# Kernel optimization log

Hardware: AMD Instinct MI355X
Metric: run time of the kernel (lower is better)

## Reference

```python
import jax, jax.numpy as jnp
import numpy as np
from jax import lax

B, T, D, H = 64, 1024, 256, 512


def setup_inputs() -> dict:
    key = jax.random.key(0)
    k1, k2, k3, k4, k5 = jax.random.split(key, 5)
    s = 1.0 / np.sqrt(H)
    return {
        "x": jax.random.normal(k1, (B, T, D), dtype=jnp.float32),
        "W_ih": jax.random.uniform(k2, (4 * H, D), minval=-s, maxval=s, dtype=jnp.float32),
        "W_hh": jax.random.uniform(k3, (4 * H, H), minval=-s, maxval=s, dtype=jnp.float32),
        "b_ih": jax.random.uniform(k4, (4 * H,), minval=-s, maxval=s, dtype=jnp.float32),
        "b_hh": jax.random.uniform(k5, (4 * H,), minval=-s, maxval=s, dtype=jnp.float32),
    }


def reference(x, W_ih, W_hh, b_ih, b_hh):
    # x: [B, T, D] -> time-major [T, B, D]
    xT = jnp.swapaxes(x, 0, 1)
    b, h_dim = x.shape[0], W_hh.shape[1]
    # Precompute input projections for all timesteps: [T, B, 4H]
    x_proj = jnp.einsum("tbd,gd->tbg", xT, W_ih) + b_ih + b_hh

    def step(carry, xg):
        h, c = carry
        gates = xg + h @ W_hh.T  # [B, 4H]
        i, f, g, o = jnp.split(gates, 4, axis=-1)
        c = jax.nn.sigmoid(f) * c + jax.nn.sigmoid(i) * jnp.tanh(g)
        h = jax.nn.sigmoid(o) * jnp.tanh(c)
        return (h, c), jax.nn.sigmoid(h)

    h0 = jnp.zeros((b, h_dim), dtype=x.dtype)
    c0 = jnp.zeros((b, h_dim), dtype=x.dtype)
    _, outs = lax.scan(step, (h0, c0), x_proj)  # outs: [T, B, H]
    # torch.cat along dim 0 over timesteps -> [T*B, H]
    return outs.reshape(-1, h_dim)
```

## Files before the change

### kernel.cpp

```cpp
#include <hip/hip_runtime.h>
#include <stdint.h>

#define T_STEPS 1024
#define BATCH   64
#define DIN     256
#define HDIM    512
#define G4      2048
#define NGRP    8
#define GWG     32
#define GB      8
#define NBUF    16

#define OFF_XCNT  0
#define OFF_ARR   128
#define OFF_BIAS  4096
#define OFF_WHH   16384
#define OFF_WIH   (16384 + G4*HDIM*2)
#define OFF_H     (OFF_WIH + G4*DIN*2)

typedef __attribute__((ext_vector_type(8))) short bf16x8;
typedef __attribute__((ext_vector_type(4))) float f32x4;

__device__ __forceinline__ unsigned short f2bf(float f) {
  union { float f; unsigned u; } v; v.f = f;
  unsigned r = v.u + 0x7FFF + ((v.u >> 16) & 1);
  return (unsigned short)(r >> 16);
}
__device__ __forceinline__ float sigm(float x)   { return 1.0f / (1.0f + __expf(-x)); }
__device__ __forceinline__ float tanh_f(float x) { return 2.0f / (1.0f + __expf(-2.0f * x)) - 1.0f; }

__global__ void k_init(unsigned char* ws) {
  int tid = blockIdx.x * blockDim.x + threadIdx.x;
  unsigned* w32 = (unsigned*)ws;
  if (tid < 512) w32[tid] = 0;
}

__global__ void k_pack(const float* __restrict__ W_ih, const float* __restrict__ W_hh,
                       const float* __restrict__ b_ih, const float* __restrict__ b_hh,
                       unsigned char* ws) {
  unsigned short* whh = (unsigned short*)(ws + OFF_WHH);
  unsigned short* wih = (unsigned short*)(ws + OFF_WIH);
  float* bias = (float*)(ws + OFF_BIAS);
  int tid = blockIdx.x * blockDim.x + threadIdx.x;
  int np = gridDim.x * blockDim.x;
  for (int i = tid; i < G4 * HDIM; i += np) whh[i] = f2bf(W_hh[i]);
  for (int i = tid; i < G4 * DIN;  i += np) wih[i] = f2bf(W_ih[i]);
  for (int i = tid; i < G4;        i += np) bias[i] = b_ih[i] + b_hh[i];
}

__device__ __forceinline__ void stage_x(const float* __restrict__ x, unsigned short* A_s,
                                        int g, int m, int c, int tstep) {
  const float* xb = x + ((size_t)(g * GB + m) * 1024 + tstep) * 256 + c * 8;
  float4 f0 = *(const float4*)(xb);
  float4 f1 = *(const float4*)(xb + 4);
  union { bf16x8 v; unsigned short s[8]; } u;
  u.s[0] = f2bf(f0.x); u.s[1] = f2bf(f0.y); u.s[2] = f2bf(f0.z); u.s[3] = f2bf(f0.w);
  u.s[4] = f2bf(f1.x); u.s[5] = f2bf(f1.y); u.s[6] = f2bf(f1.z); u.s[7] = f2bf(f1.w);
  *(bf16x8*)(A_s + m * 776 + 512 + c * 8) = u.v;
}

__global__ __launch_bounds__(256, 1) void k_lstm(unsigned char* ws,
                                                 const float* __restrict__ x,
                                                 float* __restrict__ out) {
  __shared__ __attribute__((aligned(16))) unsigned short A_s[16 * 776];
  __shared__ __attribute__((aligned(16))) unsigned short Whh_s[64 * 520];
  __shared__ __attribute__((aligned(16))) unsigned short Wih_s[64 * 264];
  __shared__ __attribute__((aligned(16))) float gl[16 * 64];
  __shared__ int s_rank;

  const int tid = threadIdx.x;

  unsigned xcc;
  asm("s_getreg_b32 %0, hwreg(HW_REG_XCC_ID)" : "=s"(xcc));
  xcc &= 7;
  unsigned* xcnt = (unsigned*)(ws + OFF_XCNT);
  if (tid == 0)
    s_rank = (int)__hip_atomic_fetch_add(&xcnt[xcc], 1u, __ATOMIC_RELAXED, __HIP_MEMORY_SCOPE_AGENT);
  __syncthreads();
  const int rank = s_rank;
  if (rank >= GWG) return;

  const int g  = (int)xcc;
  const int jt = rank;

  const unsigned short* whh_g = (const unsigned short*)(ws + OFF_WHH);
  const unsigned short* wih_g = (const unsigned short*)(ws + OFF_WIH);
  const float*          bias_g = (const float*)(ws + OFF_BIAS);
  unsigned short*       hring = (unsigned short*)(ws + OFF_H) + (size_t)g * (NBUF * GB * HDIM);
  unsigned* arrive = (unsigned*)(ws + OFF_ARR + g * 128);

  {
    int rl = tid >> 2, part = tid & 3;
    int grow = (rl >> 4) * 512 + jt * 16 + (rl & 15);
    const unsigned short* src = whh_g + grow * 512 + part * 128;
    unsigned short* dst = Whh_s + rl * 520 + part * 128;
    #pragma unroll
    for (int i = 0; i < 16; ++i) *(bf16x8*)(dst + i * 8) = *(const bf16x8*)(src + i * 8);
    const unsigned short* src2 = wih_g + grow * 256 + part * 64;
    unsigned short* dst2 = Wih_s + rl * 264 + part * 64;
    #pragma unroll
    for (int i = 0; i < 8; ++i) *(bf16x8*)(dst2 + i * 8) = *(const bf16x8*)(src2 + i * 8);
  }

  {
    unsigned* a32 = (unsigned*)A_s;
    for (int i = tid; i < 16 * 776 / 2; i += 256) a32[i] = 0;
  }

  float biasr[4];
  float c_reg = 0.f;
  const int ub = tid >> 4, jl = tid & 15;
  if (tid < 128) {
    #pragma unroll
    for (int gt = 0; gt < 4; ++gt)
      biasr[gt] = bias_g[gt * 512 + jt * 16 + jl];
  }

  const int lane = tid & 63, wave = tid >> 6;
  const int arow = lane & 15;
  const int kg   = (lane >> 4) * 8;
  const int rl   = wave * 16 + (lane & 15);
  const int sm   = tid >> 5, sc = tid & 31;

  __syncthreads();

  stage_x(x, A_s, g, sm, sc, 0);
  __syncthreads();
  f32x4 accX = {0.f, 0.f, 0.f, 0.f};
  #pragma unroll
  for (int kx = 0; kx < 8; ++kx) {
    bf16x8 a = *(const bf16x8*)(A_s + arow * 776 + 512 + kx * 32 + kg);
    bf16x8 b = *(const bf16x8*)(Wih_s + rl * 264 + kx * 32 + kg);
    accX = __builtin_amdgcn_mfma_f32_16x16x32_bf16(a, b, accX, 0, 0, 0);
  }
  __syncthreads();
  stage_x(x, A_s, g, sm, sc, 1);
  __syncthreads();

  for (int t = 0; t < T_STEPS; ++t) {
    f32x4 acc = accX;
    #pragma unroll
    for (int kk = 0; kk < 16; ++kk) {
      bf16x8 a = *(const bf16x8*)(A_s + arow * 776 + kk * 32 + kg);
      bf16x8 b = *(const bf16x8*)(Whh_s + rl * 520 + kk * 32 + kg);
      acc = __builtin_amdgcn_mfma_f32_16x16x32_bf16(a, b, acc, 0, 0, 0);
    }
    #pragma unroll
    for (int r = 0; r < 4; ++r) {
      int m = (lane >> 4) * 4 + r;
      gl[m * 64 + wave * 16 + (lane & 15)] = acc[r];
    }
    __syncthreads();

    float hv = 0.f;
    if (tid < 128) {
      float gi = gl[ub * 64 +      jl] + biasr[0];
      float gf = gl[ub * 64 + 16 + jl] + biasr[1];
      float gg = gl[ub * 64 + 32 + jl] + biasr[2];
      float go = gl[ub * 64 + 48 + jl] + biasr[3];
      float cv = sigm(gf) * c_reg + sigm(gi) * tanh_f(gg);
      c_reg = cv;
      hv = sigm(go) * tanh_f(cv);
      if (t + 1 < T_STEPS) {
        unsigned short* hd = hring + (size_t)((t + 1) & (NBUF - 1)) * (GB * HDIM);
        hd[ub * HDIM + jt * 16 + jl] = f2bf(hv);
        asm volatile("s_waitcnt vmcnt(0)" ::: "memory");
      }
    }
    __syncthreads();

    if (tid == 0 && t + 1 < T_STEPS)
      __hip_atomic_fetch_add(arrive, 1u, __ATOMIC_RELAXED, __HIP_MEMORY_SCOPE_WORKGROUP);
    if (tid < 128)
      out[((size_t)t * 64 + g * GB + ub) * 512 + jt * 16 + jl] = sigm(hv);

    if (t + 1 < T_STEPS) {
      accX = (f32x4){0.f, 0.f, 0.f, 0.f};
      #pragma unroll
      for (int kx = 0; kx < 8; ++kx) {
        bf16x8 a = *(const bf16x8*)(A_s + arow * 776 + 512 + kx * 32 + kg);
        bf16x8 b = *(const bf16x8*)(Wih_s + rl * 264 + kx * 32 + kg);
        accX = __builtin_amdgcn_mfma_f32_16x16x32_bf16(a, b, accX, 0, 0, 0);
      }
      if (tid == 0) {
        unsigned target = (unsigned)(GWG * (t + 1));
        int it = 0;
        for (;;) {
          unsigned v = __hip_atomic_fetch_or(arrive, 0x80000000u,
                                             __ATOMIC_RELAXED, __HIP_MEMORY_SCOPE_WORKGROUP);
          if ((v & 0x7FFFFFFFu) >= target) break;
          if (++it > (1 << 18)) break;
        }
      }
      __syncthreads();
      {
        const unsigned short* hs = hring + (size_t)((t + 1) & (NBUF - 1)) * (GB * HDIM)
                                 + sm * HDIM + sc * 16;
        bf16x8 h0 = *(const bf16x8*)(hs);
        bf16x8 h1 = *(const bf16x8*)(hs + 8);
        *(bf16x8*)(A_s + sm * 776 + sc * 16)     = h0;
        *(bf16x8*)(A_s + sm * 776 + sc * 16 + 8) = h1;
        if (t + 2 < T_STEPS) stage_x(x, A_s, g, sm, sc, t + 2);
      }
      __syncthreads();
    }
  }
}

extern "C" void kernel_launch(void* const* d_in, const int* in_sizes, int n_in,
                              void* d_out, int out_size, void* d_ws, size_t ws_size,
                              hipStream_t stream) {
  const float* x    = (const float*)d_in[0];
  const float* W_ih = (const float*)d_in[1];
  const float* W_hh = (const float*)d_in[2];
  const float* b_ih = (const float*)d_in[3];
  const float* b_hh = (const float*)d_in[4];
  float* out = (float*)d_out;
  unsigned char* ws = (unsigned char*)d_ws;

  hipLaunchKernelGGL(k_init, dim3(2),    dim3(256), 0, stream, ws);
  hipLaunchKernelGGL(k_pack, dim3(1024), dim3(256), 0, stream, W_ih, W_hh, b_ih, b_hh, ws);
  hipLaunchKernelGGL(k_lstm, dim3(512),  dim3(256), 0, stream, ws, x, out);
}
```

Baseline: 2.335 ms.

## Hold weights in registers with split-K waves and per-wave arrival counters

Weight fragments for W_hh and W_ih now live in registers (24 bf16x8 per lane) instead of shared memory. The K dimension is split across the four waves, each covering all four gate tiles, and the partial sums are reduced through shared memory. The barrier between issuing the h stores and arriving is removed by giving the two computing waves separate arrival counters, which a single poller checks, and the spin timeout is dropped. The goal is fewer LDS weight reads and a shorter critical path per step, at the cost of higher register pressure, an extra reduction pass, and a possible hang if a workgroup never arrives.

```diff
diff --git a/kernel.cpp b/kernel.cpp
--- a/kernel.cpp
+++ b/kernel.cpp
@@ -12,10 +12,10 @@
 #define NBUF    16
 
 #define OFF_XCNT  0
-#define OFF_ARR   128
-#define OFF_BIAS  4096
+#define OFF_ARR   1024
+#define OFF_BIAS  8192
 #define OFF_WHH   16384
-#define OFF_WIH   (16384 + G4*HDIM*2)
+#define OFF_WIH   (OFF_WHH + G4*HDIM*2)
 #define OFF_H     (OFF_WIH + G4*DIN*2)
 
 typedef __attribute__((ext_vector_type(8))) short bf16x8;
@@ -32,7 +32,7 @@
 __global__ void k_init(unsigned char* ws) {
   int tid = blockIdx.x * blockDim.x + threadIdx.x;
   unsigned* w32 = (unsigned*)ws;
-  if (tid < 512) w32[tid] = 0;
+  for (int i = tid; i < 8192 / 4; i += gridDim.x * blockDim.x) w32[i] = 0;
 }
 
 __global__ void k_pack(const float* __restrict__ W_ih, const float* __restrict__ W_hh,
@@ -63,9 +63,7 @@
                                                  const float* __restrict__ x,
                                                  float* __restrict__ out) {
   __shared__ __attribute__((aligned(16))) unsigned short A_s[16 * 776];
-  __shared__ __attribute__((aligned(16))) unsigned short Whh_s[64 * 520];
-  __shared__ __attribute__((aligned(16))) unsigned short Wih_s[64 * 264];
-  __shared__ __attribute__((aligned(16))) float gl[16 * 64];
+  __shared__ __attribute__((aligned(16))) float glp[4 * 16 * 64];
   __shared__ int s_rank;
 
   const int tid = threadIdx.x;
@@ -87,19 +85,25 @@
   const unsigned short* wih_g = (const unsigned short*)(ws + OFF_WIH);
   const float*          bias_g = (const float*)(ws + OFF_BIAS);
   unsigned short*       hring = (unsigned short*)(ws + OFF_H) + (size_t)g * (NBUF * GB * HDIM);
-  unsigned* arrive = (unsigned*)(ws + OFF_ARR + g * 128);
-
+  unsigned*             arr   = (unsigned*)(ws + OFF_ARR + g * 256);
+
+  const int lane = tid & 63, wave = tid >> 6;
+  const int arow = lane & 15;
+  const int kg   = (lane >> 4) * 8;
+  const int sm   = tid >> 5, sc = tid & 31;
+
+  bf16x8 bq[24];
   {
-    int rl = tid >> 2, part = tid & 3;
-    int grow = (rl >> 4) * 512 + jt * 16 + (rl & 15);
-    const unsigned short* src = whh_g + grow * 512 + part * 128;
-    unsigned short* dst = Whh_s + rl * 520 + part * 128;
-    #pragma unroll
-    for (int i = 0; i < 16; ++i) *(bf16x8*)(dst + i * 8) = *(const bf16x8*)(src + i * 8);
-    const unsigned short* src2 = wih_g + grow * 256 + part * 64;
-    unsigned short* dst2 = Wih_s + rl * 264 + part * 64;
-    #pragma unroll
-    for (int i = 0; i < 8; ++i) *(bf16x8*)(dst2 + i * 8) = *(const bf16x8*)(src2 + i * 8);
+    #pragma unroll
+    for (int u = 0; u < 6; ++u)
+      #pragma unroll
+      for (int nt = 0; nt < 4; ++nt) {
+        int grow = nt * 512 + jt * 16 + (lane & 15);
+        const unsigned short* src;
+        if (u < 4) src = whh_g + (size_t)grow * 512 + (wave * 4 + u) * 32 + kg;
+        else       src = wih_g + (size_t)grow * 256 + (wave * 2 + (u - 4)) * 32 + kg;
+        bq[u * 4 + nt] = *(const bf16x8*)src;
+      }
   }
 
   {
@@ -116,80 +120,90 @@
       biasr[gt] = bias_g[gt * 512 + jt * 16 + jl];
   }
 
-  const int lane = tid & 63, wave = tid >> 6;
-  const int arow = lane & 15;
-  const int kg   = (lane >> 4) * 8;
-  const int rl   = wave * 16 + (lane & 15);
-  const int sm   = tid >> 5, sc = tid & 31;
-
   __syncthreads();
 
   stage_x(x, A_s, g, sm, sc, 0);
   __syncthreads();
-  f32x4 accX = {0.f, 0.f, 0.f, 0.f};
-  #pragma unroll
-  for (int kx = 0; kx < 8; ++kx) {
-    bf16x8 a = *(const bf16x8*)(A_s + arow * 776 + 512 + kx * 32 + kg);
-    bf16x8 b = *(const bf16x8*)(Wih_s + rl * 264 + kx * 32 + kg);
-    accX = __builtin_amdgcn_mfma_f32_16x16x32_bf16(a, b, accX, 0, 0, 0);
+  f32x4 accX[4];
+  {
+    #pragma unroll
+    for (int nt = 0; nt < 4; ++nt) accX[nt] = (f32x4){0.f, 0.f, 0.f, 0.f};
+    #pragma unroll
+    for (int j = 0; j < 2; ++j) {
+      int xk = wave * 2 + j;
+      bf16x8 a = *(const bf16x8*)(A_s + arow * 776 + 512 + xk * 32 + kg);
+      #pragma unroll
+      for (int nt = 0; nt < 4; ++nt)
+        accX[nt] = __builtin_amdgcn_mfma_f32_16x16x32_bf16(a, bq[(4 + j) * 4 + nt], accX[nt], 0, 0, 0);
+    }
   }
   __syncthreads();
   stage_x(x, A_s, g, sm, sc, 1);
   __syncthreads();
 
   for (int t = 0; t < T_STEPS; ++t) {
-    f32x4 acc = accX;
-    #pragma unroll
-    for (int kk = 0; kk < 16; ++kk) {
+    f32x4 acc[4];
+    #pragma unroll
+    for (int nt = 0; nt < 4; ++nt) acc[nt] = accX[nt];
+    #pragma unroll
+    for (int u = 0; u < 4; ++u) {
+      int kk = wave * 4 + u;
       bf16x8 a = *(const bf16x8*)(A_s + arow * 776 + kk * 32 + kg);
-      bf16x8 b = *(const bf16x8*)(Whh_s + rl * 520 + kk * 32 + kg);
-      acc = __builtin_amdgcn_mfma_f32_16x16x32_bf16(a, b, acc, 0, 0, 0);
-    }
-    #pragma unroll
-    for (int r = 0; r < 4; ++r) {
-      int m = (lane >> 4) * 4 + r;
-      gl[m * 64 + wave * 16 + (lane & 15)] = acc[r];
-    }
+      #pragma unroll
+      for (int nt = 0; nt < 4; ++nt)
+        acc[nt] = __builtin_amdgcn_mfma_f32_16x16x32_bf16(a, bq[u * 4 + nt], acc[nt], 0, 0, 0);
+    }
+    #pragma unroll
+    for (int nt = 0; nt < 4; ++nt)
+      #pragma unroll
+      for (int r = 0; r < 4; ++r) {
+        int m = (lane >> 4) * 4 + r;
+        glp[wave * 1024 + m * 64 + nt * 16 + (lane & 15)] = acc[nt][r];
+      }
     __syncthreads();
 
     float hv = 0.f;
     if (tid < 128) {
-      float gi = gl[ub * 64 +      jl] + biasr[0];
-      float gf = gl[ub * 64 + 16 + jl] + biasr[1];
-      float gg = gl[ub * 64 + 32 + jl] + biasr[2];
-      float go = gl[ub * 64 + 48 + jl] + biasr[3];
-      float cv = sigm(gf) * c_reg + sigm(gi) * tanh_f(gg);
+      float gs[4];
+      #pragma unroll
+      for (int gt = 0; gt < 4; ++gt)
+        gs[gt] = glp[ub * 64 + gt * 16 + jl]
+               + glp[1024 + ub * 64 + gt * 16 + jl]
+               + glp[2048 + ub * 64 + gt * 16 + jl]
+               + glp[3072 + ub * 64 + gt * 16 + jl] + biasr[gt];
+      float cv = sigm(gs[1]) * c_reg + sigm(gs[0]) * tanh_f(gs[2]);
       c_reg = cv;
-      hv = sigm(go) * tanh_f(cv);
+      hv = sigm(gs[3]) * tanh_f(cv);
       if (t + 1 < T_STEPS) {
         unsigned short* hd = hring + (size_t)((t + 1) & (NBUF - 1)) * (GB * HDIM);
         hd[ub * HDIM + jt * 16 + jl] = f2bf(hv);
         asm volatile("s_waitcnt vmcnt(0)" ::: "memory");
-      }
-    }
-    __syncthreads();
-
-    if (tid == 0 && t + 1 < T_STEPS)
-      __hip_atomic_fetch_add(arrive, 1u, __ATOMIC_RELAXED, __HIP_MEMORY_SCOPE_WORKGROUP);
-    if (tid < 128)
+        if (lane == 0)
+          __hip_atomic_fetch_add(&arr[wave * 32], 1u,
+                                 __ATOMIC_RELAXED, __HIP_MEMORY_SCOPE_WORKGROUP);
+      }
       out[((size_t)t * 64 + g * GB + ub) * 512 + jt * 16 + jl] = sigm(hv);
+    }
 
     if (t + 1 < T_STEPS) {
-      accX = (f32x4){0.f, 0.f, 0.f, 0.f};
-      #pragma unroll
-      for (int kx = 0; kx < 8; ++kx) {
-        bf16x8 a = *(const bf16x8*)(A_s + arow * 776 + 512 + kx * 32 + kg);
-        bf16x8 b = *(const bf16x8*)(Wih_s + rl * 264 + kx * 32 + kg);
-        accX = __builtin_amdgcn_mfma_f32_16x16x32_bf16(a, b, accX, 0, 0, 0);
-      }
-      if (tid == 0) {
-        unsigned target = (unsigned)(GWG * (t + 1));
-        int it = 0;
+      #pragma unroll
+      for (int nt = 0; nt < 4; ++nt) accX[nt] = (f32x4){0.f, 0.f, 0.f, 0.f};
+      #pragma unroll
+      for (int j = 0; j < 2; ++j) {
+        int xk = wave * 2 + j;
+        bf16x8 a = *(const bf16x8*)(A_s + arow * 776 + 512 + xk * 32 + kg);
+        #pragma unroll
+        for (int nt = 0; nt < 4; ++nt)
+          accX[nt] = __builtin_amdgcn_mfma_f32_16x16x32_bf16(a, bq[(4 + j) * 4 + nt], accX[nt], 0, 0, 0);
+      }
+      if (tid == 192) {
+        const unsigned target = 32u * (unsigned)(t + 1);
         for (;;) {
-          unsigned v = __hip_atomic_fetch_or(arrive, 0x80000000u,
-                                             __ATOMIC_RELAXED, __HIP_MEMORY_SCOPE_WORKGROUP);
-          if ((v & 0x7FFFFFFFu) >= target) break;
-          if (++it > (1 << 18)) break;
+          unsigned v0 = __hip_atomic_fetch_or(&arr[0], 0x80000000u,
+                                              __ATOMIC_RELAXED, __HIP_MEMORY_SCOPE_WORKGROUP);
+          unsigned v1 = __hip_atomic_fetch_or(&arr[32], 0x80000000u,
+                                              __ATOMIC_RELAXED, __HIP_MEMORY_SCOPE_WORKGROUP);
+          if ((v0 & 0x7FFFFFFFu) >= target && (v1 & 0x7FFFFFFFu) >= target) break;
         }
       }
       __syncthreads();
@@ -218,7 +232,7 @@
   float* out = (float*)d_out;
   unsigned char* ws = (unsigned char*)d_ws;
 
-  hipLaunchKernelGGL(k_init, dim3(2),    dim3(256), 0, stream, ws);
+  hipLaunchKernelGGL(k_init, dim3(8),    dim3(256), 0, stream, ws);
   hipLaunchKernelGGL(k_pack, dim3(1024), dim3(256), 0, stream, W_ih, W_hh, b_ih, b_hh, ws);
   hipLaunchKernelGGL(k_lstm, dim3(512),  dim3(256), 0, stream, ws, x, out);
 }
```

After: 2.849 ms. 22.0% more time.
